# Kernel tuning notes

Measured on AMD Instinct MI355X. Metric: run time of the kernel, lower is better.

Reference implementation:

```python
import jax, jax.numpy as jnp
import numpy as np

MAX_REL_K = 16  # max_relative_position (keys)
MAX_REL_V = 16  # max_relative_position (values)


def _relative_positions(T, max_pos):
    # equal q/k length branch of relative_positions()
    r = jnp.arange(T)
    dist = jnp.clip(r[None, :] - r[:, None], -max_pos, max_pos)
    return dist + max_pos  # [T, T], values in [0, 2*max_pos]


def setup_inputs() -> dict:
    key = jax.random.key(0)
    ks = jax.random.split(key, 5)
    B, H, T, D = 4, 16, 1024, 64
    return {
        "q": jax.random.normal(ks[0], (B, H, T, D), dtype=jnp.float32),
        "k": jax.random.normal(ks[1], (B, H, T, D), dtype=jnp.float32),
        "v": jax.random.normal(ks[2], (B, H, T, D), dtype=jnp.float32),
        "emb_k": jax.random.normal(ks[3], (2 * MAX_REL_K + 1, D), dtype=jnp.float32),
        "emb_v": jax.random.normal(ks[4], (2 * MAX_REL_V + 1, D), dtype=jnp.float32),
    }


def reference(q, k, v, emb_k, emb_v):
    T = q.shape[2]
    D = k.shape[-1]
    rel_k = emb_k[_relative_positions(T, MAX_REL_K)]  # [T, T, D]
    rel_v = emb_v[_relative_positions(T, MAX_REL_V)]  # [T, T, D]
    # QK^T plus relative-key bias: [B, H, T, T]
    logits = jnp.einsum("bhtd,bhsd->bhts", q, k)
    logits = logits + jnp.einsum("bhtd,tsd->bhts", q, rel_k)
    logits = logits * (1.0 / jnp.sqrt(jnp.asarray(D, dtype=logits.dtype)))
    attn = jax.nn.softmax(logits, axis=-1)  # [B, H, T, T]
    out = jnp.einsum("bhts,bhsd->bhtd", attn, v)
    out = out + jnp.einsum("bhts,tsd->bhtd", attn, rel_v)
    return out, attn
```

## Files before the change

kernel.cpp:

```cpp
#include <hip/hip_runtime.h>

typedef __attribute__((ext_vector_type(8))) short short8;
typedef __attribute__((ext_vector_type(4))) float f32x4;

#define T_ 1024
#define D_ 64
#define CSC 0.18033688f

static __device__ __forceinline__ unsigned short f2bf(float f) {
    union { float f; unsigned u; } x; x.f = f;
    unsigned r = x.u + 0x7fffu + ((x.u >> 16) & 1u);
    return (unsigned short)(r >> 16);
}
static __device__ __forceinline__ float bf2f(unsigned short h) {
    union { unsigned u; float f; } x; x.u = ((unsigned)h) << 16;
    return x.f;
}
static __device__ __forceinline__ float fexp2(float x) {
    return __builtin_amdgcn_exp2f(fminf(x, 60.f));
}
static __device__ __forceinline__ void gload16(const unsigned short* g, unsigned short* l) {
    __builtin_amdgcn_global_load_lds(
        (__attribute__((address_space(1))) void*)g,
        (__attribute__((address_space(3))) void*)l, 16, 0, 0);
}

__global__ __launch_bounds__(256) void preconv(
    const float* __restrict__ kg, const float* __restrict__ vg,
    unsigned short* __restrict__ kbf, unsigned short* __restrict__ vtb)
{
    __shared__ float vt[64][65];
    const int tid = threadIdx.x;
    const int bh = blockIdx.x >> 4, tile = blockIdx.x & 15;
    const long eb = (long)bh * (T_ * D_) + tile * 64 * D_;
    const int r = tid >> 2, d0 = (tid & 3) * 16;

    {
        const float* s = kg + eb + r * 64 + d0;
        f32x4 a0 = *(const f32x4*)(s + 0);
        f32x4 a1 = *(const f32x4*)(s + 4);
        f32x4 a2 = *(const f32x4*)(s + 8);
        f32x4 a3 = *(const f32x4*)(s + 12);
        short8 p0, p1;
        #pragma unroll
        for (int i = 0; i < 4; ++i) {
            p0[i]     = (short)f2bf(a0[i]); p0[4 + i] = (short)f2bf(a1[i]);
            p1[i]     = (short)f2bf(a2[i]); p1[4 + i] = (short)f2bf(a3[i]);
        }
        *(short8*)&kbf[eb + r * 64 + d0]     = p0;
        *(short8*)&kbf[eb + r * 64 + d0 + 8] = p1;
    }
    {
        const float* s = vg + eb + r * 64 + d0;
        f32x4 a0 = *(const f32x4*)(s + 0);
        f32x4 a1 = *(const f32x4*)(s + 4);
        f32x4 a2 = *(const f32x4*)(s + 8);
        f32x4 a3 = *(const f32x4*)(s + 12);
        #pragma unroll
        for (int i = 0; i < 4; ++i) {
            vt[d0 + i][r]      = a0[i];
            vt[d0 + 4 + i][r]  = a1[i];
            vt[d0 + 8 + i][r]  = a2[i];
            vt[d0 + 12 + i][r] = a3[i];
        }
    }
    __syncthreads();
    {
        short8 p0, p1;
        #pragma unroll
        for (int i = 0; i < 8; ++i) {
            p0[i] = (short)f2bf(vt[r][d0 + i]);
            p1[i] = (short)f2bf(vt[r][d0 + 8 + i]);
        }
        const long vb = ((long)bh * D_ + r) * T_ + tile * 64 + d0;
        *(short8*)&vtb[vb]     = p0;
        *(short8*)&vtb[vb + 8] = p1;
    }
}

__global__ __launch_bounds__(256, 3) void relattn(
    const float* __restrict__ qg,
    const unsigned short* __restrict__ kbf,
    const unsigned short* __restrict__ vtb,
    const float* __restrict__ embk,
    const float* __restrict__ embv,
    float* __restrict__ outg, float* __restrict__ attng)
{
    __shared__ __align__(16) unsigned char lds[53376];
    unsigned short* QPt   = (unsigned short*)(lds);
    unsigned short* Kb    = (unsigned short*)(lds + 8192);
    unsigned short* Vb    = (unsigned short*)(lds + 24576);
    float*          biasS = (float*)(lds + 40960);
    unsigned short* wS    = (unsigned short*)(lds + 49408);
    float*          embvS = (float*)(lds);

    const int tid  = threadIdx.x;
    const int lane = tid & 63;
    const int wv   = tid >> 6;
    const int g16  = lane >> 4;
    const int l16  = lane & 15;
    const int rbase = wv * 16 + g16 * 4;

    const int lg = ((blockIdx.x & 7) << 7) | (blockIdx.x >> 3);
    const int bh = lg >> 4;
    const int t0 = (lg & 15) * 64;
    const int dtile = t0 >> 6;
    const long base = (long)bh * (T_ * D_);

    int kofs0, kofs1, vofs0, vofs1;
    {
        const int gg = lane & 7, lr = lane >> 3;
        const int r0 = (wv * 2) * 8 + lr, r1 = (wv * 2 + 1) * 8 + lr;
        kofs0 = r0 * 64   + ((gg ^ (r0 & 7)) << 3);
        kofs1 = r1 * 64   + ((gg ^ (r1 & 7)) << 3);
        vofs0 = r0 * 1024 + ((gg ^ (r0 & 7)) << 3);
        vofs1 = r1 * 1024 + ((gg ^ (r1 & 7)) << 3);
    }
    const unsigned short* kbh = kbf + base;
    const unsigned short* vbh = vtb + base;
    unsigned short* kdst = Kb + wv * 1024;
    unsigned short* vdst = Vb + wv * 1024;

    {
        const int r = tid >> 2, d0 = (tid & 3) * 16;
        const float* s = qg + base + (long)t0 * D_ + r * 64 + d0;
        f32x4 a0 = *(const f32x4*)(s + 0);
        f32x4 a1 = *(const f32x4*)(s + 4);
        f32x4 a2 = *(const f32x4*)(s + 8);
        f32x4 a3 = *(const f32x4*)(s + 12);
        short8 p0, p1;
        #pragma unroll
        for (int i = 0; i < 4; ++i) {
            p0[i]     = (short)f2bf(a0[i]); p0[4 + i] = (short)f2bf(a1[i]);
            p1[i]     = (short)f2bf(a2[i]); p1[4 + i] = (short)f2bf(a3[i]);
        }
        const int sw = (r & 7) << 3;
        *(short8*)&QPt[(r * 64 + d0)     ^ sw] = p0;
        *(short8*)&QPt[(r * 64 + d0 + 8) ^ sw] = p1;
    }
    for (int i = tid; i < 64 * 31; i += 256) wS[i] = 0;
    __syncthreads();

    gload16(kbh + kofs0, kdst);
    gload16(kbh + kofs1, kdst + 512);

    for (int p = tid; p < 64 * 33; p += 256) {
        const int r = p / 33, j = p - r * 33;
        const float* qr = qg + base + (long)(t0 + r) * D_;
        const float* er = embk + j * D_;
        float acc = 0.f;
        #pragma unroll
        for (int d = 0; d < 64; d += 4) {
            f32x4 a = *(const f32x4*)(qr + d);
            f32x4 b = *(const f32x4*)(er + d);
            acc += a[0] * b[0] + a[1] * b[1] + a[2] * b[2] + a[3] * b[3];
        }
        biasS[r * 33 + j] = acc * CSC;
    }

    short8 qfrag[2];
    {
        const int r = wv * 16 + l16;
        const int sw = (r & 7) << 3;
        qfrag[0] = *(short8*)&QPt[((r * 64 + 0  + g16 * 8) ^ sw)];
        qfrag[1] = *(short8*)&QPt[((r * 64 + 32 + g16 * 8) ^ sw)];
    }
    __syncthreads();

    float bias_m[4], bias_p[4];
    #pragma unroll
    for (int j = 0; j < 4; ++j) {
        bias_m[j] = biasS[(rbase + j) * 33 + 0];
        bias_p[j] = biasS[(rbase + j) * 33 + 32];
    }

    float zacc[4] = {0.f, 0.f, 0.f, 0.f};
    for (int tile = 0; tile < 16; ++tile) {
        unsigned short* Kc = Kb + ((tile & 1) << 12);
        if (tile < 15) {
            unsigned short* kn = Kb + (((tile + 1) & 1) << 12) + wv * 1024;
            gload16(kbh + (tile + 1) * 4096 + kofs0, kn);
            gload16(kbh + (tile + 1) * 4096 + kofs1, kn + 512);
        }
        f32x4 acc[4];
        #pragma unroll
        for (int sc = 0; sc < 4; ++sc) {
            f32x4 a = {0.f, 0.f, 0.f, 0.f};
            #pragma unroll
            for (int ks = 0; ks < 2; ++ks) {
                const int r = sc * 16 + l16;
                short8 bf = *(short8*)&Kc[((r * 64 + ks * 32 + g16 * 8) ^ ((r & 7) << 3))];
                a = __builtin_amdgcn_mfma_f32_16x16x32_bf16(qfrag[ks], bf, a, 0, 0, 0);
            }
            acc[sc] = a;
        }
        if (tile < dtile - 1) {
            #pragma unroll
            for (int j = 0; j < 4; ++j)
                #pragma unroll
                for (int sc = 0; sc < 4; ++sc)
                    zacc[j] += fexp2(fmaf(acc[sc][j], CSC, bias_m[j]));
        } else if (tile > dtile + 1) {
            #pragma unroll
            for (int j = 0; j < 4; ++j)
                #pragma unroll
                for (int sc = 0; sc < 4; ++sc)
                    zacc[j] += fexp2(fmaf(acc[sc][j], CSC, bias_p[j]));
        } else {
            #pragma unroll
            for (int j = 0; j < 4; ++j) {
                const int rl = rbase + j;
                const int tg = t0 + rl;
                #pragma unroll
                for (int sc = 0; sc < 4; ++sc) {
                    const int sg = tile * 64 + sc * 16 + l16;
                    int dsr = sg - tg;
                    int dc = dsr < -16 ? -16 : (dsr > 16 ? 16 : dsr);
                    const float b = biasS[rl * 33 + dc + 16];
                    zacc[j] += fexp2(fmaf(acc[sc][j], CSC, b));
                }
            }
        }
        __syncthreads();
    }
    float iZ[4];
    #pragma unroll
    for (int j = 0; j < 4; ++j) {
        float z = zacc[j];
        #pragma unroll
        for (int o = 1; o < 16; o <<= 1) z += __shfl_xor(z, o);
        iZ[j] = 1.f / z;
    }

    gload16(kbh + kofs0, kdst);
    gload16(kbh + kofs1, kdst + 512);
    gload16(vbh + vofs0, vdst);
    gload16(vbh + vofs1, vdst + 512);
    __syncthreads();

    f32x4 oacc[4];
    {
        f32x4 z = {0.f, 0.f, 0.f, 0.f};
        #pragma unroll
        for (int dc = 0; dc < 4; ++dc) oacc[dc] = z;
    }
    float ps0[4]  = {0.f, 0.f, 0.f, 0.f};
    float ps32[4] = {0.f, 0.f, 0.f, 0.f};
    float* attnB = attng + (long)bh * T_ * T_;

    for (int tile = 0; tile < 16; ++tile) {
        unsigned short* Kc = Kb + ((tile & 1) << 12);
        unsigned short* Vc = Vb + ((tile & 1) << 12);
        if (tile < 15) {
            unsigned short* kn = Kb + (((tile + 1) & 1) << 12) + wv * 1024;
            unsigned short* vn = Vb + (((tile + 1) & 1) << 12) + wv * 1024;
            gload16(kbh + (tile + 1) * 4096 + kofs0, kn);
            gload16(kbh + (tile + 1) * 4096 + kofs1, kn + 512);
            gload16(vbh + (tile + 1) * 64 + vofs0, vn);
            gload16(vbh + (tile + 1) * 64 + vofs1, vn + 512);
        }

        f32x4 acc[4];
        #pragma unroll
        for (int sc = 0; sc < 4; ++sc) {
            f32x4 a = {0.f, 0.f, 0.f, 0.f};
            #pragma unroll
            for (int ks = 0; ks < 2; ++ks) {
                const int r = sc * 16 + l16;
                short8 bf = *(short8*)&Kc[((r * 64 + ks * 32 + g16 * 8) ^ ((r & 7) << 3))];
                a = __builtin_amdgcn_mfma_f32_16x16x32_bf16(qfrag[ks], bf, a, 0, 0, 0);
            }
            acc[sc] = a;
        }

        if (tile < dtile - 1) {
            #pragma unroll
            for (int j = 0; j < 4; ++j) {
                const int rl = rbase + j;
                const int tg = t0 + rl;
                #pragma unroll
                for (int sc = 0; sc < 4; ++sc) {
                    const int sl = sc * 16 + l16;
                    const float a = fexp2(fmaf(acc[sc][j], CSC, bias_m[j])) * iZ[j];
                    attnB[(long)tg * T_ + tile * 64 + sl] = a;
                    QPt[((rl * 64 + sl) ^ ((rl & 7) << 3))] = f2bf(a);
                    ps0[j] += a;
                }
            }
        } else if (tile > dtile + 1) {
            #pragma unroll
            for (int j = 0; j < 4; ++j) {
                const int rl = rbase + j;
                const int tg = t0 + rl;
                #pragma unroll
                for (int sc = 0; sc < 4; ++sc) {
                    const int sl = sc * 16 + l16;
                    const float a = fexp2(fmaf(acc[sc][j], CSC, bias_p[j])) * iZ[j];
                    attnB[(long)tg * T_ + tile * 64 + sl] = a;
                    QPt[((rl * 64 + sl) ^ ((rl & 7) << 3))] = f2bf(a);
                    ps32[j] += a;
                }
            }
        } else {
            #pragma unroll
            for (int j = 0; j < 4; ++j) {
                const int rl = rbase + j;
                const int tg = t0 + rl;
                #pragma unroll
                for (int sc = 0; sc < 4; ++sc) {
                    const int sl = sc * 16 + l16;
                    const int sg = tile * 64 + sl;
                    const int dsr = sg - tg;
                    int dc = dsr < -16 ? -16 : (dsr > 16 ? 16 : dsr);
                    const float b = biasS[rl * 33 + dc + 16];
                    const float a = fexp2(fmaf(acc[sc][j], CSC, b)) * iZ[j];
                    attnB[(long)tg * T_ + sg] = a;
                    QPt[((rl * 64 + sl) ^ ((rl & 7) << 3))] = f2bf(a);
                    if (dsr <= -16)      ps0[j]  += a;
                    else if (dsr >= 16)  ps32[j] += a;
                    else                 wS[rl * 31 + dsr + 15] = f2bf(a);
                }
            }
        }

        #pragma unroll
        for (int ks = 0; ks < 2; ++ks) {
            const int rp = wv * 16 + l16;
            short8 pa = *(short8*)&QPt[((rp * 64 + ks * 32 + g16 * 8) ^ ((rp & 7) << 3))];
            #pragma unroll
            for (int dc = 0; dc < 4; ++dc) {
                const int rv = dc * 16 + l16;
                short8 vb = *(short8*)&Vc[((rv * 64 + ks * 32 + g16 * 8) ^ ((rv & 7) << 3))];
                oacc[dc] = __builtin_amdgcn_mfma_f32_16x16x32_bf16(pa, vb, oacc[dc], 0, 0, 0);
            }
        }
        __syncthreads();
    }

    for (int i = tid; i < 33 * 64; i += 256) embvS[i] = embv[i];

    float w0r[4], w32r[4];
    #pragma unroll
    for (int j = 0; j < 4; ++j) {
        float a0 = ps0[j], a2 = ps32[j];
        #pragma unroll
        for (int o = 1; o < 16; o <<= 1) {
            a0 += __shfl_xor(a0, o);
            a2 += __shfl_xor(a2, o);
        }
        w0r[j] = a0; w32r[j] = a2;
    }
    __syncthreads();

    float vals[4][4];
    #pragma unroll
    for (int j = 0; j < 4; ++j)
        #pragma unroll
        for (int dc = 0; dc < 4; ++dc)
            vals[j][dc] = oacc[dc][j]
                        + w0r[j]  * embvS[0 * 64  + dc * 16 + l16]
                        + w32r[j] * embvS[32 * 64 + dc * 16 + l16];
    for (int jj = 1; jj < 32; ++jj) {
        float e[4];
        #pragma unroll
        for (int dc = 0; dc < 4; ++dc) e[dc] = embvS[jj * 64 + dc * 16 + l16];
        #pragma unroll
        for (int j = 0; j < 4; ++j) {
            const float w = bf2f(wS[(rbase + j) * 31 + jj - 1]);
            #pragma unroll
            for (int dc = 0; dc < 4; ++dc) vals[j][dc] += w * e[dc];
        }
    }
    #pragma unroll
    for (int j = 0; j < 4; ++j) {
        const int tg = t0 + rbase + j;
        #pragma unroll
        for (int dc = 0; dc < 4; ++dc)
            outg[base + (long)tg * D_ + dc * 16 + l16] = vals[j][dc];
    }
}

static __device__ __forceinline__ void stage64x64(const float* __restrict__ src,
                                                  unsigned short* dst, int tid) {
    const int r = tid >> 2, d0 = (tid & 3) * 16;
    const float* s = src + r * 64 + d0;
    __attribute__((aligned(16))) float tmp[16];
    *(float4*)(tmp + 0)  = *(const float4*)(s + 0);
    *(float4*)(tmp + 4)  = *(const float4*)(s + 4);
    *(float4*)(tmp + 8)  = *(const float4*)(s + 8);
    *(float4*)(tmp + 12) = *(const float4*)(s + 12);
    #pragma unroll
    for (int h = 0; h < 2; ++h) {
        short8 pk;
        #pragma unroll
        for (int i = 0; i < 8; ++i) pk[i] = (short)f2bf(tmp[h * 8 + i]);
        *(short8*)&dst[((r * 64 + d0 + h * 8) ^ ((r & 7) << 3))] = pk;
    }
}
static __device__ __forceinline__ void stage64x64T(const float* __restrict__ src,
                                                   unsigned short* dst, int tid) {
    const int r = tid >> 2, d0 = (tid & 3) * 16;
    const float* s = src + r * 64 + d0;
    __attribute__((aligned(16))) float tmp[16];
    *(float4*)(tmp + 0)  = *(const float4*)(s + 0);
    *(float4*)(tmp + 4)  = *(const float4*)(s + 4);
    *(float4*)(tmp + 8)  = *(const float4*)(s + 8);
    *(float4*)(tmp + 12) = *(const float4*)(s + 12);
    #pragma unroll
    for (int i = 0; i < 16; ++i) {
        const int dd = d0 + i;
        dst[((dd * 64 + r) ^ ((dd & 7) << 3))] = f2bf(tmp[i]);
    }
}

__global__ __launch_bounds__(256, 3) void relattn_fb(
    const float* __restrict__ qg, const float* __restrict__ kg,
    const float* __restrict__ vg, const float* __restrict__ embk,
    const float* __restrict__ embv,
    float* __restrict__ outg, float* __restrict__ attng)
{
    __shared__ __align__(16) unsigned short QPt[64 * 64];
    __shared__ __align__(16) unsigned short Kt[64 * 64];
    __shared__ __align__(16) unsigned short Vt[64 * 64];
    __shared__ float biasS[64 * 34];
    __shared__ float wS[64 * 33];
    __shared__ float embvS[33 * 64];

    const int tid  = threadIdx.x;
    const int lane = tid & 63;
    const int wv   = tid >> 6;
    const int g16  = lane >> 4;
    const int l16  = lane & 15;
    const int rbase = wv * 16 + g16 * 4;

    const int lg = ((blockIdx.x & 7) << 7) | (blockIdx.x >> 3);
    const int bh = lg >> 4;
    const int t0 = (lg & 15) * 64;
    const int dtile = t0 >> 6;
    const long base = (long)bh * (T_ * D_);

    stage64x64(qg + base + (long)t0 * D_, QPt, tid);
    for (int i = tid; i < 33 * 64; i += 256) embvS[i] = embv[i];
    for (int i = tid; i < 64 * 33; i += 256) wS[i] = 0.f;
    __syncthreads();

    for (int p = tid; p < 64 * 33; p += 256) {
        const int r = p / 33, j = p - r * 33;
        const float* qr = qg + base + (long)(t0 + r) * D_;
        const float* er = embk + j * D_;
        float acc = 0.f;
        #pragma unroll
        for (int d = 0; d < 64; d += 4) {
            f32x4 a = *(const f32x4*)(qr + d);
            f32x4 b = *(const f32x4*)(er + d);
            acc += a[0] * b[0] + a[1] * b[1] + a[2] * b[2] + a[3] * b[3];
        }
        biasS[r * 34 + j] = acc * CSC;
    }
    short8 qfrag[2];
    {
        const int r = wv * 16 + l16;
        const int sw = (r & 7) << 3;
        qfrag[0] = *(short8*)&QPt[((r * 64 + 0  + g16 * 8) ^ sw)];
        qfrag[1] = *(short8*)&QPt[((r * 64 + 32 + g16 * 8) ^ sw)];
    }
    __syncthreads();

    float bias_m[4], bias_p[4];
    #pragma unroll
    for (int j = 0; j < 4; ++j) {
        bias_m[j] = biasS[(rbase + j) * 34 + 0];
        bias_p[j] = biasS[(rbase + j) * 34 + 32];
    }

    float zacc[4] = {0.f, 0.f, 0.f, 0.f};
    for (int tile = 0; tile < 16; ++tile) {
        stage64x64(kg + base + (long)tile * 64 * D_, Kt, tid);
        __syncthreads();
        f32x4 acc[4];
        #pragma unroll
        for (int sc = 0; sc < 4; ++sc) {
            f32x4 a = {0.f, 0.f, 0.f, 0.f};
            #pragma unroll
            for (int ks = 0; ks < 2; ++ks) {
                const int r = sc * 16 + l16;
                short8 bf = *(short8*)&Kt[((r * 64 + ks * 32 + g16 * 8) ^ ((r & 7) << 3))];
                a = __builtin_amdgcn_mfma_f32_16x16x32_bf16(qfrag[ks], bf, a, 0, 0, 0);
            }
            acc[sc] = a;
        }
        if (tile < dtile - 1) {
            #pragma unroll
            for (int j = 0; j < 4; ++j)
                #pragma unroll
                for (int sc = 0; sc < 4; ++sc)
                    zacc[j] += fexp2(fmaf(acc[sc][j], CSC, bias_m[j]));
        } else if (tile > dtile + 1) {
            #pragma unroll
            for (int j = 0; j < 4; ++j)
                #pragma unroll
                for (int sc = 0; sc < 4; ++sc)
                    zacc[j] += fexp2(fmaf(acc[sc][j], CSC, bias_p[j]));
        } else {
            #pragma unroll
            for (int j = 0; j < 4; ++j) {
                const int rl = rbase + j;
                const int tg = t0 + rl;
                #pragma unroll
                for (int sc = 0; sc < 4; ++sc) {
                    const int sg = tile * 64 + sc * 16 + l16;
                    int dsr = sg - tg;
                    int dc = dsr < -16 ? -16 : (dsr > 16 ? 16 : dsr);
                    zacc[j] += fexp2(fmaf(acc[sc][j], CSC, biasS[rl * 34 + dc + 16]));
                }
            }
        }
        __syncthreads();
    }
    float iZ[4];
    #pragma unroll
    for (int j = 0; j < 4; ++j) {
        float z = zacc[j];
        #pragma unroll
        for (int o = 1; o < 16; o <<= 1) z += __shfl_xor(z, o);
        iZ[j] = 1.f / z;
    }

    f32x4 oacc[4];
    {
        f32x4 z = {0.f, 0.f, 0.f, 0.f};
        #pragma unroll
        for (int dc = 0; dc < 4; ++dc) oacc[dc] = z;
    }
    float ps0[4]  = {0.f, 0.f, 0.f, 0.f};
    float ps32[4] = {0.f, 0.f, 0.f, 0.f};
    float* attnB = attng + (long)bh * T_ * T_;

    for (int tile = 0; tile < 16; ++tile) {
        stage64x64 (kg + base + (long)tile * 64 * D_, Kt, tid);
        stage64x64T(vg + base + (long)tile * 64 * D_, Vt, tid);
        __syncthreads();
        f32x4 acc[4];
        #pragma unroll
        for (int sc = 0; sc < 4; ++sc) {
            f32x4 a = {0.f, 0.f, 0.f, 0.f};
            #pragma unroll
            for (int ks = 0; ks < 2; ++ks) {
                const int r = sc * 16 + l16;
                short8 bf = *(short8*)&Kt[((r * 64 + ks * 32 + g16 * 8) ^ ((r & 7) << 3))];
                a = __builtin_amdgcn_mfma_f32_16x16x32_bf16(qfrag[ks], bf, a, 0, 0, 0);
            }
            acc[sc] = a;
        }
        #pragma unroll
        for (int j = 0; j < 4; ++j) {
            const int rl = rbase + j;
            const int tg = t0 + rl;
            #pragma unroll
            for (int sc = 0; sc < 4; ++sc) {
                const int sl = sc * 16 + l16;
                const int sg = tile * 64 + sl;
                const int dsr = sg - tg;
                int dc = dsr < -16 ? -16 : (dsr > 16 ? 16 : dsr);
                const float b = biasS[rl * 34 + dc + 16];
                const float a = fexp2(fmaf(acc[sc][j], CSC, b)) * iZ[j];
                attnB[(long)tg * T_ + sg] = a;
                QPt[((rl * 64 + sl) ^ ((rl & 7) << 3))] = f2bf(a);
                if (dsr <= -16)      ps0[j]  += a;
                else if (dsr >= 16)  ps32[j] += a;
                else                 wS[rl * 33 + dsr + 16] = a;
            }
        }
        #pragma unroll
        for (int ks = 0; ks < 2; ++ks) {
            const int rp = wv * 16 + l16;
            short8 pa = *(short8*)&QPt[((rp * 64 + ks * 32 + g16 * 8) ^ ((rp & 7) << 3))];
            #pragma unroll
            for (int dc = 0; dc < 4; ++dc) {
                const int rv = dc * 16 + l16;
                short8 vb = *(short8*)&Vt[((rv * 64 + ks * 32 + g16 * 8) ^ ((rv & 7) << 3))];
                oacc[dc] = __builtin_amdgcn_mfma_f32_16x16x32_bf16(pa, vb, oacc[dc], 0, 0, 0);
            }
        }
        __syncthreads();
    }

    float w0r[4], w32r[4];
    #pragma unroll
    for (int j = 0; j < 4; ++j) {
        float a0 = ps0[j], a2 = ps32[j];
        #pragma unroll
        for (int o = 1; o < 16; o <<= 1) {
            a0 += __shfl_xor(a0, o);
            a2 += __shfl_xor(a2, o);
        }
        w0r[j] = a0; w32r[j] = a2;
    }
    __syncthreads();

    float vals[4][4];
    #pragma unroll
    for (int j = 0; j < 4; ++j)
        #pragma unroll
        for (int dc = 0; dc < 4; ++dc)
            vals[j][dc] = oacc[dc][j]
                        + w0r[j]  * embvS[0 * 64  + dc * 16 + l16]
                        + w32r[j] * embvS[32 * 64 + dc * 16 + l16];
    for (int jj = 1; jj < 32; ++jj) {
        float e[4];
        #pragma unroll
        for (int dc = 0; dc < 4; ++dc) e[dc] = embvS[jj * 64 + dc * 16 + l16];
        #pragma unroll
        for (int j = 0; j < 4; ++j) {
            const float w = wS[(rbase + j) * 33 + jj];
            #pragma unroll
            for (int dc = 0; dc < 4; ++dc) vals[j][dc] += w * e[dc];
        }
    }
    #pragma unroll
    for (int j = 0; j < 4; ++j) {
        const int tg = t0 + rbase + j;
        #pragma unroll
        for (int dc = 0; dc < 4; ++dc)
            outg[base + (long)tg * D_ + dc * 16 + l16] = vals[j][dc];
    }
}

extern "C" void kernel_launch(void* const* d_in, const int* in_sizes, int n_in,
                              void* d_out, int out_size, void* d_ws, size_t ws_size,
                              hipStream_t stream) {
    const float* q    = (const float*)d_in[0];
    const float* k    = (const float*)d_in[1];
    const float* v    = (const float*)d_in[2];
    const float* embk = (const float*)d_in[3];
    const float* embv = (const float*)d_in[4];
    float* out  = (float*)d_out;
    float* attn = out + (long)4 * 16 * 1024 * 64;

    if (ws_size >= (size_t)16777216) {
        unsigned short* kbf = (unsigned short*)d_ws;
        unsigned short* vtb = kbf + 4194304;
        preconv<<<dim3(1024), dim3(256), 0, stream>>>(k, v, kbf, vtb);
        relattn<<<dim3(1024), dim3(256), 0, stream>>>(q, kbf, vtb, embk, embv, out, attn);
    } else {
        relattn_fb<<<dim3(1024), dim3(256), 0, stream>>>(q, k, v, embk, embv, out, attn);
    }
}
```

Before: 169.3 us.

## Shrink LDS footprint to fit four blocks per CU by single-buffering V

```diff
diff --git a/kernel.cpp b/kernel.cpp
--- a/kernel.cpp
+++ b/kernel.cpp
@@ -11,10 +11,6 @@
     union { float f; unsigned u; } x; x.f = f;
     unsigned r = x.u + 0x7fffu + ((x.u >> 16) & 1u);
     return (unsigned short)(r >> 16);
-}
-static __device__ __forceinline__ float bf2f(unsigned short h) {
-    union { unsigned u; float f; } x; x.u = ((unsigned)h) << 16;
-    return x.f;
 }
 static __device__ __forceinline__ float fexp2(float x) {
     return __builtin_amdgcn_exp2f(fminf(x, 60.f));
@@ -78,7 +74,7 @@
     }
 }
 
-__global__ __launch_bounds__(256, 3) void relattn(
+__global__ __launch_bounds__(256, 4) void relattn(
     const float* __restrict__ qg,
     const unsigned short* __restrict__ kbf,
     const unsigned short* __restrict__ vtb,
@@ -86,12 +82,12 @@
     const float* __restrict__ embv,
     float* __restrict__ outg, float* __restrict__ attng)
 {
-    __shared__ __align__(16) unsigned char lds[53376];
+    __shared__ __align__(16) unsigned char lds[40960];
     unsigned short* QPt   = (unsigned short*)(lds);
     unsigned short* Kb    = (unsigned short*)(lds + 8192);
-    unsigned short* Vb    = (unsigned short*)(lds + 24576);
-    float*          biasS = (float*)(lds + 40960);
-    unsigned short* wS    = (unsigned short*)(lds + 49408);
+    unsigned short* Vt    = (unsigned short*)(lds + 24576);
+    _Float16*       biasH = (_Float16*)(lds + 32768);
+    _Float16*       wS    = (_Float16*)(lds + 36992);
     float*          embvS = (float*)(lds);
 
     const int tid  = threadIdx.x;
@@ -119,7 +115,7 @@
     const unsigned short* kbh = kbf + base;
     const unsigned short* vbh = vtb + base;
     unsigned short* kdst = Kb + wv * 1024;
-    unsigned short* vdst = Vb + wv * 1024;
+    unsigned short* vdst = Vt + wv * 1024;
 
     {
         const int r = tid >> 2, d0 = (tid & 3) * 16;
@@ -138,7 +134,7 @@
         *(short8*)&QPt[(r * 64 + d0)     ^ sw] = p0;
         *(short8*)&QPt[(r * 64 + d0 + 8) ^ sw] = p1;
     }
-    for (int i = tid; i < 64 * 31; i += 256) wS[i] = 0;
+    for (int i = tid; i < 64 * 31; i += 256) wS[i] = (_Float16)0.f;
     __syncthreads();
 
     gload16(kbh + kofs0, kdst);
@@ -155,7 +151,7 @@
             f32x4 b = *(const f32x4*)(er + d);
             acc += a[0] * b[0] + a[1] * b[1] + a[2] * b[2] + a[3] * b[3];
         }
-        biasS[r * 33 + j] = acc * CSC;
+        biasH[r * 33 + j] = (_Float16)(acc * CSC);
     }
 
     short8 qfrag[2];
@@ -170,8 +166,8 @@
     float bias_m[4], bias_p[4];
     #pragma unroll
     for (int j = 0; j < 4; ++j) {
-        bias_m[j] = biasS[(rbase + j) * 33 + 0];
-        bias_p[j] = biasS[(rbase + j) * 33 + 32];
+        bias_m[j] = (float)biasH[(rbase + j) * 33 + 0];
+        bias_p[j] = (float)biasH[(rbase + j) * 33 + 32];
     }
 
     float zacc[4] = {0.f, 0.f, 0.f, 0.f};
@@ -216,7 +212,7 @@
                     const int sg = tile * 64 + sc * 16 + l16;
                     int dsr = sg - tg;
                     int dc = dsr < -16 ? -16 : (dsr > 16 ? 16 : dsr);
-                    const float b = biasS[rl * 33 + dc + 16];
+                    const float b = (float)biasH[rl * 33 + dc + 16];
                     zacc[j] += fexp2(fmaf(acc[sc][j], CSC, b));
                 }
             }
@@ -234,8 +230,6 @@
 
     gload16(kbh + kofs0, kdst);
     gload16(kbh + kofs1, kdst + 512);
-    gload16(vbh + vofs0, vdst);
-    gload16(vbh + vofs1, vdst + 512);
     __syncthreads();
 
     f32x4 oacc[4];
@@ -250,14 +244,12 @@
 
     for (int tile = 0; tile < 16; ++tile) {
         unsigned short* Kc = Kb + ((tile & 1) << 12);
-        unsigned short* Vc = Vb + ((tile & 1) << 12);
+        gload16(vbh + tile * 64 + vofs0, vdst);
+        gload16(vbh + tile * 64 + vofs1, vdst + 512);
         if (tile < 15) {
             unsigned short* kn = Kb + (((tile + 1) & 1) << 12) + wv * 1024;
-            unsigned short* vn = Vb + (((tile + 1) & 1) << 12) + wv * 1024;
             gload16(kbh + (tile + 1) * 4096 + kofs0, kn);
             gload16(kbh + (tile + 1) * 4096 + kofs1, kn + 512);
-            gload16(vbh + (tile + 1) * 64 + vofs0, vn);
-            gload16(vbh + (tile + 1) * 64 + vofs1, vn + 512);
         }
 
         f32x4 acc[4];
@@ -312,16 +304,18 @@
                     const int sg = tile * 64 + sl;
                     const int dsr = sg - tg;
                     int dc = dsr < -16 ? -16 : (dsr > 16 ? 16 : dsr);
-                    const float b = biasS[rl * 33 + dc + 16];
+                    const float b = (float)biasH[rl * 33 + dc + 16];
                     const float a = fexp2(fmaf(acc[sc][j], CSC, b)) * iZ[j];
                     attnB[(long)tg * T_ + sg] = a;
                     QPt[((rl * 64 + sl) ^ ((rl & 7) << 3))] = f2bf(a);
                     if (dsr <= -16)      ps0[j]  += a;
                     else if (dsr >= 16)  ps32[j] += a;
-                    else                 wS[rl * 31 + dsr + 15] = f2bf(a);
+                    else                 wS[rl * 31 + dsr + 15] = (_Float16)a;
                 }
             }
         }
+
+        __syncthreads();
 
         #pragma unroll
         for (int ks = 0; ks < 2; ++ks) {
@@ -330,10 +324,11 @@
             #pragma unroll
             for (int dc = 0; dc < 4; ++dc) {
                 const int rv = dc * 16 + l16;
-                short8 vb = *(short8*)&Vc[((rv * 64 + ks * 32 + g16 * 8) ^ ((rv & 7) << 3))];
+                short8 vb = *(short8*)&Vt[((rv * 64 + ks * 32 + g16 * 8) ^ ((rv & 7) << 3))];
                 oacc[dc] = __builtin_amdgcn_mfma_f32_16x16x32_bf16(pa, vb, oacc[dc], 0, 0, 0);
             }
         }
+
         __syncthreads();
     }
 
@@ -366,7 +361,7 @@
         for (int dc = 0; dc < 4; ++dc) e[dc] = embvS[jj * 64 + dc * 16 + l16];
         #pragma unroll
         for (int j = 0; j < 4; ++j) {
-            const float w = bf2f(wS[(rbase + j) * 31 + jj - 1]);
+            const float w = (float)wS[(rbase + j) * 31 + jj - 1];
             #pragma unroll
             for (int dc = 0; dc < 4; ++dc) vals[j][dc] += w * e[dc];
         }
```

After: 182.8 us. +7.9%, slower.
